# Performance work log

Measured on AMD Instinct MI355X. Metric: run time of the kernel, lower is better.

Reference implementation:

```python
import jax, jax.numpy as jnp
import numpy as np
from jax.scipy.special import logsumexp

VOCAB, EMB, HID, K = 50000, 256, 512, 48
H = HID // 2
B, T = 64, 512


def setup_inputs() -> dict:
    key = jax.random.key(0)
    ks = jax.random.split(key, 15)
    f = lambda k, s: jax.random.normal(k, s, jnp.float32) * 0.1
    return {
        "x": jax.random.randint(ks[0], (B, T), 0, VOCAB),
        "tags": jax.random.randint(ks[1], (B, T), 0, K),
        "mask": jnp.ones((B, T), jnp.bool_),
        "emb": f(ks[2], (VOCAB, EMB)),
        "Wih_f": f(ks[3], (4 * H, EMB)),
        "Whh_f": f(ks[4], (4 * H, H)),
        "b_f": f(ks[5], (4 * H,)),
        "Wih_b": f(ks[6], (4 * H, EMB)),
        "Whh_b": f(ks[7], (4 * H, H)),
        "b_b": f(ks[8], (4 * H,)),
        "fc_W": f(ks[9], (K, HID)),
        "fc_b": f(ks[10], (K,)),
        "start_t": f(ks[11], (K,)),
        "end_t": f(ks[12], (K,)),
        "trans": f(ks[13], (K, K)),
    }


def _lstm_dir(xs, Wih, Whh, b, reverse):
    # xs: [S, N, E]; scan over axis 0 (PyTorch gate order i,f,g,o; bias = b_ih+b_hh)
    n = xs.shape[1]
    hdim = Whh.shape[1]

    def step(carry, x_t):
        h, c = carry
        gates = x_t @ Wih.T + h @ Whh.T + b
        i, fg, g, o = jnp.split(gates, 4, axis=-1)
        i = jax.nn.sigmoid(i)
        fg = jax.nn.sigmoid(fg)
        g = jnp.tanh(g)
        o = jax.nn.sigmoid(o)
        c = fg * c + i * g
        h = o * jnp.tanh(c)
        return (h, c), h

    init = (jnp.zeros((n, hdim), xs.dtype), jnp.zeros((n, hdim), xs.dtype))
    _, hs = jax.lax.scan(step, init, xs, reverse=reverse)
    return hs


def _crf_nll(emissions, tags, mask, start_t, end_t, trans):
    # torchcrf with batch_first=True, reduction='mean'; returns -llh.mean()
    em = jnp.transpose(emissions, (1, 0, 2))  # [T,B,K] time-major
    tg = tags.T                                # [T,B]
    m = mask.T.astype(em.dtype)                # [T,B]
    bidx = jnp.arange(em.shape[1])

    # numerator: score of the gold tag path
    emit = jnp.take_along_axis(em, tg[..., None], axis=-1)[..., 0]  # [T,B]
    tr = trans[tg[:-1], tg[1:]]                                      # [T-1,B]
    num = start_t[tg[0]] + emit[0] + jnp.sum((tr + emit[1:]) * m[1:], axis=0)
    last = (jnp.sum(mask, axis=1) - 1).astype(jnp.int32)             # [B]
    num = num + end_t[tg[last, bidx]]

    # denominator: forward algorithm (sequential logsumexp recurrence)
    def step(alpha, inp):
        e_t, m_t = inp
        nxt = logsumexp(alpha[:, :, None] + trans[None] + e_t[:, None, :], axis=1)
        return jnp.where(m_t[:, None] > 0, nxt, alpha), None

    alpha0 = start_t + em[0]                     # [B,K]
    alpha, _ = jax.lax.scan(step, alpha0, (em[1:], m[1:]))
    den = logsumexp(alpha + end_t, axis=-1)      # [B]
    return -jnp.mean(num - den)


def reference(x, tags, mask, emb, Wih_f, Whh_f, b_f, Wih_b, Whh_b, b_b, fc_W, fc_b, start_t, end_t, trans):
    table = emb.at[0].set(0.0)  # padding_idx=0 row is zero
    e = table[x]                # [B,T,EMB]
    # Faithful to source: batch-first embeds fed into a seq-first nn.LSTM,
    # so the recurrence runs over axis 0 (the data batch axis).
    h_f = _lstm_dir(e, Wih_f, Whh_f, b_f, False)
    h_b = _lstm_dir(e, Wih_b, Whh_b, b_b, True)
    lstm_out = jnp.concatenate([h_f, h_b], axis=-1)  # [B,T,HID]
    emissions = lstm_out @ fc_W.T + fc_b             # [B,T,K]
    return _crf_nll(emissions, tags, mask, start_t, end_t, trans)
```

## Files before the change

### kernel.cpp

```cpp
#include <hip/hip_runtime.h>
#include <hip/hip_bf16.h>

#define VOCAB 50000
#define EMBD 256
#define HIDD 512
#define KTAG 48
#define HD 256
#define BB 64
#define TT 512
#define GATES 1024

typedef __bf16 bf16x8 __attribute__((ext_vector_type(8)));
typedef float f32x4 __attribute__((ext_vector_type(4)));

#define GLDS16(gp, lp) __builtin_amdgcn_global_load_lds( \
    (const __attribute__((address_space(1))) void*)(gp), \
    (__attribute__((address_space(3))) void*)(lp), 16, 0, 0)

__device__ __forceinline__ f32x4 mfma16(bf16x8 a, bf16x8 b, f32x4 c){
  return __builtin_amdgcn_mfma_f32_16x16x32_bf16(a, b, c, 0, 0, 0);
}
__device__ __forceinline__ float fsig(float x){
  return __builtin_amdgcn_rcpf(1.0f + __expf(-x));
}
__device__ __forceinline__ float ftanh(float x){
  x = fminf(10.0f, fmaxf(-10.0f, x));
  float e = __expf(2.0f*x);
  return (e - 1.0f) * __builtin_amdgcn_rcpf(e + 1.0f);
}

__global__ __launch_bounds__(256) void convert_all(
    const float* emb, const float* wf, const float* wb,
    const float* uf, const float* ub, const float* fc,
    __bf16* o_emb, __bf16* o_wih, __bf16* o_whf, __bf16* o_whb, __bf16* o_fc){
  const long U_emb = (long)VOCAB*EMBD/8;
  const long U_w   = 1024L*256/8;
  const long U_fc  = 48L*512/8;
  const long total = U_emb + 4*U_w + U_fc;
  long u = (long)blockIdx.x*256 + threadIdx.x;
  if (u >= total) return;
  const float* src; __bf16* dst; long j; bool zro = false;
  if (u < U_emb){ src = emb; dst = o_emb; j = u; zro = (u < EMBD/8); }
  else if (u < U_emb +   U_w){ j = u - U_emb;           src = wf; dst = o_wih; }
  else if (u < U_emb + 2*U_w){ j = u - U_emb -   U_w;   src = wb; dst = o_wih + 262144; }
  else if (u < U_emb + 3*U_w){ j = u - U_emb - 2*U_w;   src = uf; dst = o_whf; }
  else if (u < U_emb + 4*U_w){ j = u - U_emb - 3*U_w;   src = ub; dst = o_whb; }
  else                       { j = u - U_emb - 4*U_w;   src = fc; dst = o_fc;  }
  const float4 a  = *(const float4*)(src + j*8);
  const float4 b2 = *(const float4*)(src + j*8 + 4);
  union { __bf16 h[8]; uint4 v; } pk;
  pk.h[0]=(__bf16)(zro?0.f:a.x);  pk.h[1]=(__bf16)(zro?0.f:a.y);
  pk.h[2]=(__bf16)(zro?0.f:a.z);  pk.h[3]=(__bf16)(zro?0.f:a.w);
  pk.h[4]=(__bf16)(zro?0.f:b2.x); pk.h[5]=(__bf16)(zro?0.f:b2.y);
  pk.h[6]=(__bf16)(zro?0.f:b2.z); pk.h[7]=(__bf16)(zro?0.f:b2.w);
  *(uint4*)(dst + j*8) = pk.v;
}

__global__ __launch_bounds__(256) void gemm_pre(const int* x, const __bf16* embb,
                                                const __bf16* wih, const float* bf,
                                                const float* bb2, __bf16* pre){
  __shared__ __attribute__((aligned(16))) __bf16 As[2][128*32];
  __shared__ __attribute__((aligned(16))) __bf16 Bs[2][128*32];
  const int bid = blockIdx.x;
  const int bm = bid >> 4, bn = bid & 15;
  const int m0 = bm*128, n0 = bn*128;
  const int tid = threadIdx.x, l = tid & 63, w = tid >> 6;
  const int lr = l & 15, lk = l >> 4;
  const int wm = w >> 1, wn = w & 1;
  f32x4 acc[4][4];
  #pragma unroll
  for (int a=0;a<4;a++) for (int b3=0;b3<4;b3++) acc[a][b3] = (f32x4){0.f,0.f,0.f,0.f};

  const __bf16* agp[2];
  const __bf16* bgp[2];
  #pragma unroll
  for (int c=0;c<2;c++){
    const int id = w*2 + c;
    const int slot = id*64 + l;
    const int r = slot >> 2, kk = (slot & 3)*8;
    const int idx = x[m0 + r];
    agp[c] = embb + (size_t)idx*EMBD + kk;
    bgp[c] = wih + (size_t)(n0 + r)*EMBD + kk;
  }

  auto stage = [&](int buf, int k0){
    #pragma unroll
    for (int c=0;c<2;c++){
      const int id = w*2 + c;
      GLDS16(agp[c] + k0, &As[buf][id*512]);
      GLDS16(bgp[c] + k0, &Bs[buf][id*512]);
    }
  };

  stage(0, 0);
  int cur = 0;
  #pragma unroll 1
  for (int it = 0; it < 8; it++){
    __syncthreads();
    if (it < 7) stage(cur^1, (it+1)*32);
    bf16x8 af[4], bfr[4];
    #pragma unroll
    for (int mt=0;mt<4;mt++) af[mt] = *(const bf16x8*)(&As[cur][(wm*64 + mt*16 + lr)*32 + lk*8]);
    #pragma unroll
    for (int nt=0;nt<4;nt++) bfr[nt] = *(const bf16x8*)(&Bs[cur][(wn*64 + nt*16 + lr)*32 + lk*8]);
    #pragma unroll
    for (int mt=0;mt<4;mt++)
      #pragma unroll
      for (int nt=0;nt<4;nt++)
        acc[mt][nt] = mfma16(af[mt], bfr[nt], acc[mt][nt]);
    cur ^= 1;
  }
  #pragma unroll
  for (int mt=0;mt<4;mt++)
    #pragma unroll
    for (int nt=0;nt<4;nt++){
      const int col = n0 + wn*64 + nt*16 + lr;
      const float bv = (col < GATES) ? bf[col] : bb2[col - GATES];
      #pragma unroll
      for (int r=0;r<4;r++){
        const int row = m0 + wm*64 + mt*16 + lk*4 + r;
        pre[(size_t)row*2048 + col] = (__bf16)(acc[mt][nt][r] + bv);
      }
    }
}

__global__ __launch_bounds__(512) void lstm_rec(const __bf16* whhF, const __bf16* whhB,
                                                const __bf16* pre, __bf16* hcat){
  __shared__ __attribute__((aligned(16))) __bf16 wbuf[2][32768];
  __shared__ __attribute__((aligned(16))) __bf16 hLDS[16*264];
  const int bid = blockIdx.x;
  const int dir = bid & 1, tg = bid >> 1;
  const int t0 = tg*16;
  const int tid = threadIdx.x, l = tid & 63, w = tid >> 6;
  const int lr = l & 15, lk = l >> 4;
  const __bf16* whh = dir ? whhB : whhF;

  {
    const bf16x8 z = (bf16x8){0,0,0,0,0,0,0,0};
    *(bf16x8*)(&hLDS[tid*8]) = z;
    if (tid < 16) *(bf16x8*)(&hLDS[(512+tid)*8]) = z;
  }

  auto stageR = [&](int par, int r){
    #pragma unroll
    for (int o = 0; o < 8; o++){
      const __bf16* g = whh + (size_t)(w*128 + o*16 + (l>>2))*HD + r*32 + (l&3)*8;
      GLDS16(g, &wbuf[par][w*4096 + o*512]);
    }
  };
  __bf16 pv[4][2][4];
  auto loadPV = [&](int bs){
    #pragma unroll
    for (int q=0;q<4;q++)
      #pragma unroll
      for (int j=0;j<2;j++)
        #pragma unroll
        for (int r=0;r<4;r++)
          pv[q][j][r] = pre[(size_t)(bs*TT + t0 + lk*4 + r)*2048 + dir*GATES
                            + q*256 + w*32 + j*16 + lr];
  };

  float cst[2][4];
  #pragma unroll
  for (int j=0;j<2;j++)
    #pragma unroll
    for (int r=0;r<4;r++) cst[j][r] = 0.f;

  stageR(0, 0);
  loadPV(dir ? (BB-1) : 0);
  int prev_b = 0;

  #pragma unroll 1
  for (int s = 0; s < BB; s++){
    const int bs = dir ? (BB-1-s) : s;
    f32x4 acc[4][2];
    #pragma unroll
    for (int q=0;q<4;q++)
      #pragma unroll
      for (int j=0;j<2;j++) acc[q][j] = (f32x4){0.f,0.f,0.f,0.f};

    #pragma unroll
    for (int r = 0; r < 8; r++){
      __syncthreads();
      if (r == 0 && s > 0){
        const int row = tid >> 5, ch = tid & 31;
        bf16x8 hv = *(const bf16x8*)(&hLDS[row*264 + ch*8]);
        *(bf16x8*)(&hcat[((size_t)prev_b*TT + t0 + row)*HIDD + dir*HD + ch*8]) = hv;
      }
      stageR((r+1)&1, (r+1)&7);
      bf16x8 a = *(const bf16x8*)(&hLDS[lr*264 + r*32 + lk*8]);
      #pragma unroll
      for (int q=0;q<4;q++)
        #pragma unroll
        for (int j=0;j<2;j++){
          const int row = q*256 + w*32 + j*16 + lr;
          bf16x8 bb = *(const bf16x8*)(&wbuf[r&1][row*32 + lk*8]);
          acc[q][j] = mfma16(a, bb, acc[q][j]);
        }
    }

    asm volatile("s_waitcnt lgkmcnt(0)" ::: "memory");
    __builtin_amdgcn_s_barrier();
    asm volatile("" ::: "memory");

    #pragma unroll
    for (int j=0;j<2;j++){
      #pragma unroll
      for (int r=0;r<4;r++){
        float gi = acc[0][j][r] + (float)pv[0][j][r];
        float gf = acc[1][j][r] + (float)pv[1][j][r];
        float gg = acc[2][j][r] + (float)pv[2][j][r];
        float go = acc[3][j][r] + (float)pv[3][j][r];
        float iv=fsig(gi), fv=fsig(gf), gv=ftanh(gg), ov=fsig(go);
        float cn = fv*cst[j][r] + iv*gv;
        cst[j][r] = cn;
        hLDS[(lk*4+r)*264 + w*32 + j*16 + lr] = (__bf16)(ov*ftanh(cn));
      }
    }
    if (s < BB-1) loadPV(dir ? (BB-2-s) : (s+1));
    asm volatile("s_waitcnt lgkmcnt(0)" ::: "memory");
    __builtin_amdgcn_s_barrier();
    asm volatile("" ::: "memory");
    prev_b = bs;
  }
  {
    const int row = tid >> 5, ch = tid & 31;
    bf16x8 hv = *(const bf16x8*)(&hLDS[row*264 + ch*8]);
    *(bf16x8*)(&hcat[((size_t)prev_b*TT + t0 + row)*HIDD + dir*HD + ch*8]) = hv;
  }
}

__global__ __launch_bounds__(256) void gemm_emis(const __bf16* hcat, const __bf16* fcw,
                                                 const float* fcb, float* emis){
  const int tid = threadIdx.x, l = tid & 63, w = tid >> 6;
  const int lr = l & 15, lk = l >> 4;
  const size_t m0 = (size_t)blockIdx.x*64 + w*16;
  f32x4 acc[3];
  #pragma unroll
  for (int nt=0;nt<3;nt++) acc[nt] = (f32x4){0.f,0.f,0.f,0.f};
  #pragma unroll
  for (int kt=0; kt<16; kt++){
    bf16x8 a = *(const bf16x8*)(&hcat[(m0 + lr)*HIDD + kt*32 + lk*8]);
    #pragma unroll
    for (int nt=0;nt<3;nt++){
      bf16x8 b = *(const bf16x8*)(&fcw[(size_t)(nt*16 + lr)*HIDD + kt*32 + lk*8]);
      acc[nt] = mfma16(a, b, acc[nt]);
    }
  }
  #pragma unroll
  for (int nt=0;nt<3;nt++){
    const int col = nt*16 + lr;
    const float bv = fcb[col];
    #pragma unroll
    for (int r=0;r<4;r++){
      const size_t row = m0 + lk*4 + r;
      emis[row*KTAG + col] = acc[nt][r] + bv;
    }
  }
}

__global__ __launch_bounds__(64) void crf_num(const int* tags, const float* emis,
                                              const float* trans, const float* start_t,
                                              const float* end_t, float* numv){
  const int b = blockIdx.x, l = threadIdx.x;
  float part = 0.f;
  for (int t = l; t < TT; t += 64){
    const int tg = tags[b*TT + t];
    const float e = emis[(size_t)(b*TT + t)*KTAG + tg];
    if (t > 0){
      const int tp = tags[b*TT + t - 1];
      part += trans[tp*KTAG + tg] + e;
    } else {
      part += start_t[tg] + e;
    }
  }
  #pragma unroll
  for (int off=32; off; off >>= 1) part += __shfl_down(part, off);
  if (l == 0){
    const int tl = tags[b*TT + TT - 1];
    numv[b] = part + end_t[tl];
  }
}

__global__ __launch_bounds__(64) void crf_den(const float* emis, const float* trans,
                                              const float* start_t, const float* end_t,
                                              float* denv){
  __shared__ float wlds[64];
  const int b = blockIdx.x, l = threadIdx.x;
  float E[48];
  #pragma unroll
  for (int j=0;j<48;j++) E[j] = (l < KTAG) ? __expf(trans[j*KTAG + l]) : 0.f;
  float alpha = (l < KTAG) ? (start_t[l] + emis[(size_t)(b*TT)*KTAG + l]) : -1e30f;
  float m = 0.f;

  float em_cur = (l < KTAG) ? emis[(size_t)(b*TT + 1)*KTAG + l] : 0.f;
  #pragma unroll 1
  for (int t = 1; t < TT; t++){
    float em_nxt = (l < KTAG && t < TT-1) ? emis[(size_t)(b*TT + t + 1)*KTAG + l] : 0.f;
    if (((t-1) & 7) == 0){
      float mm = alpha;
      #pragma unroll
      for (int off=32; off; off >>= 1) mm = fmaxf(mm, __shfl_xor(mm, off));
      m = mm;
    }
    const float wv = __expf(alpha - m);
    wlds[l] = wv;
    asm volatile("s_waitcnt lgkmcnt(0)" ::: "memory");
    float s0=0.f, s1=0.f, s2=0.f, s3=0.f;
    #pragma unroll
    for (int j=0;j<48;j+=16){
      const float4 wa = *(const float4*)(&wlds[j]);
      const float4 wb = *(const float4*)(&wlds[j+4]);
      const float4 wc = *(const float4*)(&wlds[j+8]);
      const float4 wd = *(const float4*)(&wlds[j+12]);
      s0 += wa.x*E[j]    + wa.y*E[j+1]  + wa.z*E[j+2]  + wa.w*E[j+3];
      s1 += wb.x*E[j+4]  + wb.y*E[j+5]  + wb.z*E[j+6]  + wb.w*E[j+7];
      s2 += wc.x*E[j+8]  + wc.y*E[j+9]  + wc.z*E[j+10] + wc.w*E[j+11];
      s3 += wd.x*E[j+12] + wd.y*E[j+13] + wd.z*E[j+14] + wd.w*E[j+15];
    }
    asm volatile("" ::: "memory");
    const float s = (s0 + s1) + (s2 + s3);
    alpha = (l < KTAG) ? (em_cur + m + __logf(s)) : -1e30f;
    em_cur = em_nxt;
  }
  float v = (l < KTAG) ? (alpha + end_t[l]) : -1e30f;
  float mf = v;
  #pragma unroll
  for (int off=32; off; off >>= 1) mf = fmaxf(mf, __shfl_xor(mf, off));
  float sv = __expf(v - mf);
  #pragma unroll
  for (int off=32; off; off >>= 1) sv += __shfl_xor(sv, off);
  if (l == 0) denv[b] = mf + __logf(sv);
}

__global__ __launch_bounds__(64) void finalize(const float* numv, const float* denv, float* out){
  const int l = threadIdx.x;
  float v = numv[l] - denv[l];
  #pragma unroll
  for (int off=32; off; off >>= 1) v += __shfl_down(v, off);
  if (l == 0) out[0] = -v * (1.0f/64.0f);
}

extern "C" void kernel_launch(void* const* d_in, const int* in_sizes, int n_in,
                              void* d_out, int out_size, void* d_ws, size_t ws_size,
                              hipStream_t stream){
  const int*   x     = (const int*)d_in[0];
  const int*   tags  = (const int*)d_in[1];
  const float* emb   = (const float*)d_in[3];
  const float* wih_f = (const float*)d_in[4];
  const float* whh_f = (const float*)d_in[5];
  const float* b_f   = (const float*)d_in[6];
  const float* wih_b = (const float*)d_in[7];
  const float* whh_b = (const float*)d_in[8];
  const float* b_b   = (const float*)d_in[9];
  const float* fc_W  = (const float*)d_in[10];
  const float* fc_b  = (const float*)d_in[11];
  const float* start_t = (const float*)d_in[12];
  const float* end_t   = (const float*)d_in[13];
  const float* trans   = (const float*)d_in[14];

  constexpr size_t SZ_EMBB = (size_t)VOCAB*EMBD*2;
  constexpr size_t SZ_WIH  = (size_t)2048*256*2;
  constexpr size_t SZ_WHH  = (size_t)1024*256*2;
  constexpr size_t SZ_FCW  = (size_t)48*512*2;
  constexpr size_t SZ_PRE  = (size_t)32768*2048*2;
  constexpr size_t SZ_HCAT = (size_t)32768*512*2;
  constexpr size_t SZ_EMIS = (size_t)32768*48*4;
  constexpr size_t TOTAL = SZ_EMBB + SZ_WIH + 2*SZ_WHH + SZ_FCW + SZ_PRE + SZ_HCAT + SZ_EMIS + 512;
  if (ws_size < TOTAL){ hipMemsetAsync(d_out, 0, sizeof(float), stream); return; }

  char* ws = (char*)d_ws;
  size_t off = 0;
  __bf16* embb  = (__bf16*)(ws + off); off += SZ_EMBB;
  __bf16* wihb  = (__bf16*)(ws + off); off += SZ_WIH;
  __bf16* whhfb = (__bf16*)(ws + off); off += SZ_WHH;
  __bf16* whhbb = (__bf16*)(ws + off); off += SZ_WHH;
  __bf16* fcwb  = (__bf16*)(ws + off); off += SZ_FCW;
  __bf16* pre   = (__bf16*)(ws + off); off += SZ_PRE;
  __bf16* hcat  = (__bf16*)(ws + off); off += SZ_HCAT;
  float*  emis  = (float*)(ws + off);  off += SZ_EMIS;
  float*  numv  = (float*)(ws + off);  off += 256;
  float*  denv  = (float*)(ws + off);

  convert_all<<<6774, 256, 0, stream>>>(emb, wih_f, wih_b, whh_f, whh_b, fc_W,
                                        embb, wihb, whhfb, whhbb, fcwb);
  gemm_pre<<<4096, 256, 0, stream>>>(x, embb, wihb, b_f, b_b, pre);
  lstm_rec<<<64, 512, 0, stream>>>(whhfb, whhbb, pre, hcat);
  gemm_emis<<<512, 256, 0, stream>>>(hcat, fcwb, fc_b, emis);
  crf_num<<<64, 64, 0, stream>>>(tags, emis, trans, start_t, end_t, numv);
  crf_den<<<64, 64, 0, stream>>>(emis, trans, start_t, end_t, denv);
  finalize<<<1, 64, 0, stream>>>(numv, denv, (float*)d_out);
}
```

Before: 929.3 us.

## Stream LSTM recurrent weights into registers and stage gate preactivations via LDS

The recurrent LSTM kernel drops from 512 to 256 threads per block. Each wave now loads its slice of Whh directly from global memory into a register double buffer, instead of staging all of Whh through a shared-memory double buffer with a barrier each k-chunk. Gate preactivations for the next step are async-copied into a double-buffered LDS area, h is written straight to hcat, and step 0 is peeled because it needs no matmul. This removes the per-chunk barriers and LDS traffic for the weights. In exchange it uses far more registers and repeats global/L2 weight reads every timestep with fewer waves to hide latency.

```diff
diff --git a/kernel.cpp b/kernel.cpp
--- a/kernel.cpp
+++ b/kernel.cpp
@@ -124,9 +124,18 @@
     }
 }
 
-__global__ __launch_bounds__(512) void lstm_rec(const __bf16* whhF, const __bf16* whhB,
-                                                const __bf16* pre, __bf16* hcat){
-  __shared__ __attribute__((aligned(16))) __bf16 wbuf[2][32768];
+#define LOADB(BUF, rr) do { \
+  _Pragma("unroll") \
+  for (int q_=0;q_<4;q_++){ \
+    _Pragma("unroll") \
+    for (int j_=0;j_<4;j_++){ \
+      BUF[q_*4+j_] = *(const bf16x8*)(wbp[q_][j_] + (rr)*32); } } } while(0)
+
+#define PVROW 1544
+
+__global__ __launch_bounds__(256, 1) void lstm_rec(const __bf16* whhF, const __bf16* whhB,
+                                                   const __bf16* pre, __bf16* hcat){
+  __shared__ __attribute__((aligned(16))) __bf16 pvLDS[2][16*PVROW];
   __shared__ __attribute__((aligned(16))) __bf16 hLDS[16*264];
   const int bid = blockIdx.x;
   const int dir = bid & 1, tg = bid >> 1;
@@ -135,98 +144,114 @@
   const int lr = l & 15, lk = l >> 4;
   const __bf16* whh = dir ? whhB : whhF;
 
+  const __bf16* wbp[4][4];
+  #pragma unroll
+  for (int q=0;q<4;q++)
+    #pragma unroll
+    for (int j=0;j<4;j++)
+      wbp[q][j] = whh + (size_t)(q*256 + w*64 + j*16 + lr)*HD + lk*8;
+
+  auto STAGEPV = [&](int buf, int bs){
+    #pragma unroll
+    for (int c=0;c<8;c++){
+      const int id = w*8 + c;
+      const int row = id >> 1, half = id & 1;
+      GLDS16(pre + ((size_t)bs*TT + t0 + row)*2048 + dir*GATES + half*512 + l*8,
+             &pvLDS[buf][row*PVROW + half*512]);
+    }
+  };
+
+  bf16x8 bufA[16], bufB[16];
+  float cst[4][4];
+  #pragma unroll
+  for (int j=0;j<4;j++)
+    #pragma unroll
+    for (int r=0;r<4;r++) cst[j][r] = 0.f;
+
+  STAGEPV(0, dir ? (BB-1) : 0);
+  __syncthreads();
   {
-    const bf16x8 z = (bf16x8){0,0,0,0,0,0,0,0};
-    *(bf16x8*)(&hLDS[tid*8]) = z;
-    if (tid < 16) *(bf16x8*)(&hLDS[(512+tid)*8]) = z;
-  }
-
-  auto stageR = [&](int par, int r){
-    #pragma unroll
-    for (int o = 0; o < 8; o++){
-      const __bf16* g = whh + (size_t)(w*128 + o*16 + (l>>2))*HD + r*32 + (l&3)*8;
-      GLDS16(g, &wbuf[par][w*4096 + o*512]);
-    }
-  };
-  __bf16 pv[4][2][4];
-  auto loadPV = [&](int bs){
+    const int bs = dir ? (BB-1) : 0;
+    #pragma unroll
+    for (int j=0;j<4;j++)
+      #pragma unroll
+      for (int rg=0;rg<4;rg++){
+        const int row = lk*4+rg, col = w*64 + j*16 + lr;
+        float gi = (float)pvLDS[0][row*PVROW +       col];
+        float gf = (float)pvLDS[0][row*PVROW + 256 + col];
+        float gg = (float)pvLDS[0][row*PVROW + 512 + col];
+        float go = (float)pvLDS[0][row*PVROW + 768 + col];
+        float iv=fsig(gi), fv=fsig(gf), gv=ftanh(gg), ov=fsig(go);
+        float cn = fv*cst[j][rg] + iv*gv;
+        cst[j][rg] = cn;
+        __bf16 hv = (__bf16)(ov*ftanh(cn));
+        hLDS[row*264 + col] = hv;
+        hcat[((size_t)bs*TT + t0 + row)*HIDD + dir*HD + col] = hv;
+      }
+  }
+  STAGEPV(1, dir ? (BB-2) : 1);
+  LOADB(bufA, 0);
+  LOADB(bufB, 1);
+  asm volatile("s_waitcnt lgkmcnt(0)" ::: "memory");
+  __builtin_amdgcn_s_barrier();
+  __builtin_amdgcn_sched_barrier(0);
+
+  #pragma unroll 1
+  for (int s = 1; s < BB; s++){
+    const int bs = dir ? (BB-1-s) : s;
+    f32x4 acc[4][4];
     #pragma unroll
     for (int q=0;q<4;q++)
       #pragma unroll
-      for (int j=0;j<2;j++)
+      for (int j=0;j<4;j++) acc[q][j] = (f32x4){0.f,0.f,0.f,0.f};
+
+    #pragma unroll
+    for (int r=0;r<8;r++){
+      bf16x8 a = *(const bf16x8*)(&hLDS[lr*264 + r*32 + lk*8]);
+      if ((r & 1) == 0){
         #pragma unroll
-        for (int r=0;r<4;r++)
-          pv[q][j][r] = pre[(size_t)(bs*TT + t0 + lk*4 + r)*2048 + dir*GATES
-                            + q*256 + w*32 + j*16 + lr];
-  };
-
-  float cst[2][4];
-  #pragma unroll
-  for (int j=0;j<2;j++)
-    #pragma unroll
-    for (int r=0;r<4;r++) cst[j][r] = 0.f;
-
-  stageR(0, 0);
-  loadPV(dir ? (BB-1) : 0);
-  int prev_b = 0;
-
-  #pragma unroll 1
-  for (int s = 0; s < BB; s++){
-    const int bs = dir ? (BB-1-s) : s;
-    f32x4 acc[4][2];
-    #pragma unroll
-    for (int q=0;q<4;q++)
-      #pragma unroll
-      for (int j=0;j<2;j++) acc[q][j] = (f32x4){0.f,0.f,0.f,0.f};
-
-    #pragma unroll
-    for (int r = 0; r < 8; r++){
-      __syncthreads();
-      if (r == 0 && s > 0){
-        const int row = tid >> 5, ch = tid & 31;
-        bf16x8 hv = *(const bf16x8*)(&hLDS[row*264 + ch*8]);
-        *(bf16x8*)(&hcat[((size_t)prev_b*TT + t0 + row)*HIDD + dir*HD + ch*8]) = hv;
+        for (int q=0;q<4;q++)
+          #pragma unroll
+          for (int j=0;j<4;j++)
+            acc[q][j] = mfma16(a, bufA[q*4+j], acc[q][j]);
+        if (r < 6) LOADB(bufA, r+2);
+      } else {
+        #pragma unroll
+        for (int q=0;q<4;q++)
+          #pragma unroll
+          for (int j=0;j<4;j++)
+            acc[q][j] = mfma16(a, bufB[q*4+j], acc[q][j]);
+        if (r < 6) LOADB(bufB, r+2);
       }
-      stageR((r+1)&1, (r+1)&7);
-      bf16x8 a = *(const bf16x8*)(&hLDS[lr*264 + r*32 + lk*8]);
-      #pragma unroll
-      for (int q=0;q<4;q++)
-        #pragma unroll
-        for (int j=0;j<2;j++){
-          const int row = q*256 + w*32 + j*16 + lr;
-          bf16x8 bb = *(const bf16x8*)(&wbuf[r&1][row*32 + lk*8]);
-          acc[q][j] = mfma16(a, bb, acc[q][j]);
-        }
-    }
-
+    }
+    __syncthreads();
+    if (s < BB-1){
+      STAGEPV((s+1)&1, dir ? (BB-2-s) : (s+1));
+      LOADB(bufA, 0);
+      LOADB(bufB, 1);
+    }
+    __builtin_amdgcn_sched_barrier(0);
+
+    const int pvb = s & 1;
+    #pragma unroll
+    for (int j=0;j<4;j++)
+      #pragma unroll
+      for (int rg=0;rg<4;rg++){
+        const int row = lk*4+rg, col = w*64 + j*16 + lr;
+        float gi = acc[0][j][rg] + (float)pvLDS[pvb][row*PVROW +       col];
+        float gf = acc[1][j][rg] + (float)pvLDS[pvb][row*PVROW + 256 + col];
+        float gg = acc[2][j][rg] + (float)pvLDS[pvb][row*PVROW + 512 + col];
+        float go = acc[3][j][rg] + (float)pvLDS[pvb][row*PVROW + 768 + col];
+        float iv=fsig(gi), fv=fsig(gf), gv=ftanh(gg), ov=fsig(go);
+        float cn = fv*cst[j][rg] + iv*gv;
+        cst[j][rg] = cn;
+        __bf16 hv = (__bf16)(ov*ftanh(cn));
+        hLDS[row*264 + col] = hv;
+        hcat[((size_t)bs*TT + t0 + row)*HIDD + dir*HD + col] = hv;
+      }
     asm volatile("s_waitcnt lgkmcnt(0)" ::: "memory");
     __builtin_amdgcn_s_barrier();
-    asm volatile("" ::: "memory");
-
-    #pragma unroll
-    for (int j=0;j<2;j++){
-      #pragma unroll
-      for (int r=0;r<4;r++){
-        float gi = acc[0][j][r] + (float)pv[0][j][r];
-        float gf = acc[1][j][r] + (float)pv[1][j][r];
-        float gg = acc[2][j][r] + (float)pv[2][j][r];
-        float go = acc[3][j][r] + (float)pv[3][j][r];
-        float iv=fsig(gi), fv=fsig(gf), gv=ftanh(gg), ov=fsig(go);
-        float cn = fv*cst[j][r] + iv*gv;
-        cst[j][r] = cn;
-        hLDS[(lk*4+r)*264 + w*32 + j*16 + lr] = (__bf16)(ov*ftanh(cn));
-      }
-    }
-    if (s < BB-1) loadPV(dir ? (BB-2-s) : (s+1));
-    asm volatile("s_waitcnt lgkmcnt(0)" ::: "memory");
-    __builtin_amdgcn_s_barrier();
-    asm volatile("" ::: "memory");
-    prev_b = bs;
-  }
-  {
-    const int row = tid >> 5, ch = tid & 31;
-    bf16x8 hv = *(const bf16x8*)(&hLDS[row*264 + ch*8]);
-    *(bf16x8*)(&hcat[((size_t)prev_b*TT + t0 + row)*HIDD + dir*HD + ch*8]) = hv;
+    __builtin_amdgcn_sched_barrier(0);
   }
 }
 
@@ -385,7 +410,7 @@
   convert_all<<<6774, 256, 0, stream>>>(emb, wih_f, wih_b, whh_f, whh_b, fc_W,
                                         embb, wihb, whhfb, whhbb, fcwb);
   gemm_pre<<<4096, 256, 0, stream>>>(x, embb, wihb, b_f, b_b, pre);
-  lstm_rec<<<64, 512, 0, stream>>>(whhfb, whhbb, pre, hcat);
+  lstm_rec<<<64, 256, 0, stream>>>(whhfb, whhbb, pre, hcat);
   gemm_emis<<<512, 256, 0, stream>>>(hcat, fcwb, fc_b, emis);
   crf_num<<<64, 64, 0, stream>>>(tags, emis, trans, start_t, end_t, numv);
   crf_den<<<64, 64, 0, stream>>>(emis, trans, start_t, end_t, denv);
```

Result: slower. 1.522 ms (+63.8%).
